# Performance work log

Hardware: AMD Instinct MI355X
Metric: run time of the kernel (lower is better)

Reference implementation:

```python
import jax, jax.numpy as jnp
import numpy as np

EMBED = 1024
HEADS = 16
HEAD_DIM = EMBED // HEADS


def setup_inputs() -> dict:
    key = jax.random.key(0)
    ks = jax.random.split(key, 8)
    b, t, d = 2, 2048, EMBED
    s = 1.0 / np.sqrt(d)
    return {
        'k': jax.random.normal(ks[0], (b, t, d), jnp.float32),
        'q': jax.random.normal(ks[1], (b, t, d), jnp.float32),
        'v': jax.random.normal(ks[2], (b, t, d), jnp.float32),
        'Wk': jax.random.normal(ks[3], (d, d), jnp.float32) * s,
        'Wq': jax.random.normal(ks[4], (d, d), jnp.float32) * s,
        'Wv': jax.random.normal(ks[5], (d, d), jnp.float32) * s,
        'Wo': jax.random.normal(ks[6], (d, d), jnp.float32) * s,
        'bo': jax.random.normal(ks[7], (d,), jnp.float32) * 0.01,
    }


def reference(k, q, v, Wk, Wq, Wv, Wo, bo):
    b, t, d = q.shape
    h, n = HEADS, HEAD_DIM
    # projections (q_prj bias=False, k/v bias=False per add_bias_kv=False)
    keys = (k @ Wk.T).reshape(b, t, h, n).transpose(0, 2, 1, 3)      # b h t n
    queries = (q @ Wq.T).reshape(b, t, h, n).transpose(0, 2, 1, 3)
    values = (v @ Wv.T).reshape(b, t, h, n).transpose(0, 2, 1, 3)
    att = jnp.einsum('bhtn,bhsn->bhts', queries, keys)               # b h t t
    att = jax.nn.softmax(att / np.sqrt(n), axis=-1)
    out = jnp.einsum('bhts,bhsn->bhtn', att, values)                 # b h t n
    out = out.transpose(0, 2, 1, 3).reshape(b, t, d)                 # b t (h n)
    return out @ Wo.T + bo
```

## Files before the change

### kernel.cpp

```cpp
#include <hip/hip_runtime.h>
#include <hip/hip_bf16.h>


typedef unsigned short u16;
typedef unsigned int   u32;
using short8 = __attribute__((ext_vector_type(8))) short;
using f32x4  = __attribute__((ext_vector_type(4))) float;

__device__ __forceinline__ u16 f2b(float f) {
    u32 u = __float_as_uint(f);
    u += 0x7FFFu + ((u >> 16) & 1u);
    return (u16)(u >> 16);
}
__device__ __forceinline__ u32 pack2(float lo, float hi) {
    union { __hip_bfloat162 h; u32 u; } c;
    c.h = __float22bfloat162_rn(make_float2(lo, hi));
    return c.u;
}
__device__ __forceinline__ float fexp2(float x) {
    return __builtin_amdgcn_exp2f(x);
}
__device__ __forceinline__ void gld_lds16(const u16* g, u16* l) {
    __builtin_amdgcn_global_load_lds(
        (const __attribute__((address_space(1))) void*)g,
        (__attribute__((address_space(3))) void*)l, 16, 0, 0);
}

__global__ __launch_bounds__(256) void convert_kernel(
    const float* s0, const float* s1, const float* s2, const float* s3,
    const float* s4, const float* s5, const float* s6,
    u16* d0, u16* d1, u16* d2, u16* d3, u16* d4, u16* d5, u16* d6)
{
    const int y = blockIdx.y;
    const float* s; u16* d; u32 n;
    switch (y) {
        case 0: s = s0; d = d0; n = 1048576; break;
        case 1: s = s1; d = d1; n = 1048576; break;
        case 2: s = s2; d = d2; n = 1048576; break;
        case 3: s = s3; d = d3; n = 262144; break;
        case 4: s = s4; d = d4; n = 262144; break;
        case 5: s = s5; d = d5; n = 262144; break;
        default: s = s6; d = d6; n = 262144; break;
    }
    for (u32 i = blockIdx.x * 256 + threadIdx.x; i < n; i += 256 * 1024) {
        float4 f = ((const float4*)s)[i];
        uint2 o; o.x = pack2(f.x, f.y); o.y = pack2(f.z, f.w);
        ((uint2*)d)[i] = o;
    }
}

template <int MODE>
__device__ __forceinline__ void gemm_core(
    const u16* __restrict__ A, const u16* __restrict__ B,
    void* __restrict__ C, const float* __restrict__ bias, float scale,
    u32 bm, u32 bn)
{
    constexpr u32 K = 1024;
    __shared__ u16 As[128 * 32];
    __shared__ u16 Bs[128 * 32];

    const int tid  = threadIdx.x;
    const int lane = tid & 63;
    const int w    = tid >> 6;
    const int wr   = w >> 1, wc = w & 1;
    const int ml   = lane & 15, g = lane >> 4;

    f32x4 acc[4][4] = {};

    const u32 srow = w * 32 + (lane >> 2);
    const u32 scol = (u32)(((lane & 3) ^ ((lane >> 3) & 3)) * 8);
    const u16* gA = A + (size_t)(bm + srow) * K + scol;
    const u16* gB = B + (size_t)(bn + srow) * K + scol;
    u16* lA = &As[w * 1024];
    u16* lB = &Bs[w * 1024];

    const u32 fsw = (u32)((g ^ ((ml >> 1) & 3)) * 8);

    for (u32 k0 = 0; k0 < K; k0 += 32) {
        __syncthreads();
        gld_lds16(gA + k0, lA);
        gld_lds16(gA + 16 * K + k0, lA + 512);
        gld_lds16(gB + k0, lB);
        gld_lds16(gB + 16 * K + k0, lB + 512);
        __syncthreads();

        short8 af[4], bf[4];
#pragma unroll
        for (int it = 0; it < 4; ++it)
            af[it] = *(const short8*)&As[(wr * 64 + it * 16 + ml) * 32 + fsw];
#pragma unroll
        for (int ct = 0; ct < 4; ++ct)
            bf[ct] = *(const short8*)&Bs[(wc * 64 + ct * 16 + ml) * 32 + fsw];
#pragma unroll
        for (int it = 0; it < 4; ++it)
#pragma unroll
            for (int ct = 0; ct < 4; ++ct)
                acc[it][ct] = __builtin_amdgcn_mfma_f32_16x16x32_bf16(
                    af[it], bf[ct], acc[it][ct], 0, 0, 0);
    }

    if (MODE == 3) {
#pragma unroll
        for (int ct = 0; ct < 4; ++ct) {
            const u32 col = bn + wc * 64 + ct * 16 + ml;
            u16* dst = (u16*)C + (col >> 11) * 2097152 + (col & 2047);
#pragma unroll
            for (int it = 0; it < 4; ++it) {
                const u32 row = bm + wr * 64 + it * 16 + g * 4;
#pragma unroll
                for (int r = 0; r < 4; ++r)
                    dst[(size_t)(row + r) * 2048] = f2b(acc[it][ct][r]);
            }
        }
    } else {
#pragma unroll
        for (int ct = 0; ct < 4; ++ct) {
            const u32 col = bn + wc * 64 + ct * 16 + ml;
            const float bv = (MODE == 2 && bias) ? bias[col] : 0.0f;
#pragma unroll
            for (int it = 0; it < 4; ++it) {
                const u32 row = bm + wr * 64 + it * 16 + g * 4;
#pragma unroll
                for (int r = 0; r < 4; ++r) {
                    const float v = acc[it][ct][r] * scale + bv;
                    if (MODE == 2) ((float*)C)[(size_t)(row + r) * 1024 + col] = v;
                    else           ((u16*)C)[(size_t)(row + r) * 1024 + col] = f2b(v);
                }
            }
        }
    }
}

__global__ __launch_bounds__(256) void proj3_kernel(
    const u16* kb, const u16* qb, const u16* vb,
    const u16* Wkb, const u16* Wqb, const u16* Wvb,
    u16* Kp, u16* Qp, u16* Vt)
{
    if (blockIdx.z == 0)
        gemm_core<0>(kb, Wkb, Kp, nullptr, 1.0f, blockIdx.y * 128, blockIdx.x * 128);
    else if (blockIdx.z == 1)
        gemm_core<0>(qb, Wqb, Qp, nullptr, 0.18033688011112042f, blockIdx.y * 128, blockIdx.x * 128);
    else
        gemm_core<3>(Wvb, vb, Vt, nullptr, 1.0f, blockIdx.x * 128, blockIdx.y * 128);
}

__global__ __launch_bounds__(256) void out_gemm_kernel(
    const u16* __restrict__ A, const u16* __restrict__ W,
    float* __restrict__ C, const float* __restrict__ bias)
{
    constexpr u32 K = 1024;
    __shared__ u16 As[64 * 32];
    __shared__ u16 Bs[128 * 32];

    const int tid  = threadIdx.x;
    const int lane = tid & 63;
    const int w    = tid >> 6;
    const int wr   = w >> 1, wc = w & 1;
    const int ml   = lane & 15, g = lane >> 4;
    const u32 bm   = blockIdx.y * 64, bn = blockIdx.x * 128;

    f32x4 acc[2][4] = {};

    const u32 scol = (u32)(((lane & 3) ^ ((lane >> 3) & 3)) * 8);
    const u16* gA = A + (size_t)(bm + w * 16 + (lane >> 2)) * K + scol;
    const u16* gB = W + (size_t)(bn + w * 32 + (lane >> 2)) * K + scol;
    u16* lA = &As[w * 512];
    u16* lB = &Bs[w * 1024];

    const u32 fsw = (u32)((g ^ ((ml >> 1) & 3)) * 8);

    for (u32 k0 = 0; k0 < K; k0 += 32) {
        __syncthreads();
        gld_lds16(gA + k0, lA);
        gld_lds16(gB + k0, lB);
        gld_lds16(gB + 16 * K + k0, lB + 512);
        __syncthreads();

        short8 af[2], bf[4];
#pragma unroll
        for (int it = 0; it < 2; ++it)
            af[it] = *(const short8*)&As[(wr * 32 + it * 16 + ml) * 32 + fsw];
#pragma unroll
        for (int ct = 0; ct < 4; ++ct)
            bf[ct] = *(const short8*)&Bs[(wc * 64 + ct * 16 + ml) * 32 + fsw];
#pragma unroll
        for (int it = 0; it < 2; ++it)
#pragma unroll
            for (int ct = 0; ct < 4; ++ct)
                acc[it][ct] = __builtin_amdgcn_mfma_f32_16x16x32_bf16(
                    af[it], bf[ct], acc[it][ct], 0, 0, 0);
    }

#pragma unroll
    for (int ct = 0; ct < 4; ++ct) {
        const u32 col = bn + wc * 64 + ct * 16 + ml;
        const float bv = bias ? bias[col] : 0.0f;
#pragma unroll
        for (int it = 0; it < 2; ++it) {
            const u32 row = bm + wr * 32 + it * 16 + g * 4;
#pragma unroll
            for (int r = 0; r < 4; ++r)
                C[(size_t)(row + r) * 1024 + col] = acc[it][ct][r] + bv;
        }
    }
}

__global__ __launch_bounds__(512, 4) void attn_kernel(
    const u16* __restrict__ Qp, const u16* __restrict__ Kp,
    const u16* __restrict__ Vt, u16* __restrict__ Op)
{
    __shared__ u16   Ks[2 * 4096];
    __shared__ u16   Vs[2 * 4096];
    __shared__ u16   Ps[8 * 1280];
    __shared__ float Ls[4][32];

    const int tid  = threadIdx.x;
    const int lane = tid & 63;
    const int w    = tid >> 6;
    const int wq   = w >> 1;
    const int ws   = w & 1;
    const int ml   = lane & 15;
    const int g    = lane >> 4;

    const u32 fid  = blockIdx.x + (blockIdx.y << 4);
    const u32 swz  = (fid & 7) * 64 + (fid >> 3);
    const u32 bh   = swz >> 4;
    const u32 t0   = (swz & 15) * 128;
    const u32 b    = bh >> 4, h = bh & 15;

    const u32 base  = b * 2048 * 1024 + h * 64;
    const u32 vbase = bh * 64 * 2048;

    short8 bq[2][2];
#pragma unroll
    for (int qt = 0; qt < 2; ++qt) {
        const u16* qr = Qp + base + (t0 + wq * 32 + qt * 16 + ml) * 1024 + g * 8;
        bq[qt][0] = *(const short8*)qr;
        bq[qt][1] = *(const short8*)(qr + 32);
    }

    f32x4 oacc[4][2] = {};
    float l4[2] = {};

    const u32 srow = (u32)(lane >> 3);
    const u32 schk = (u32)((lane & 7) ^ (lane >> 3));
    const u16* gK = Kp + base + (size_t)(w * 8 + srow) * 1024 + schk * 8;
    const u16* gV = Vt + vbase + (size_t)(w * 8 + srow) * 2048 + schk * 8;
    u16* lK0 = &Ks[w * 512];
    u16* lK1 = &Ks[4096 + w * 512];
    u16* lV0 = &Vs[w * 512];
    u16* lV1 = &Vs[4096 + w * 512];

    const u32 kaOff = (u32)((ws * 32 + ml) * 64 + ((g ^ (ml & 7)) * 8));
    const u32 vaOff = (u32)(ml * 64 + (((ws * 4 + g) ^ (ml & 7)) * 8));
    u16* Pw  = &Ps[w * 1280];
    u32* PwU = (u32*)Pw;
    const u32 pWr = (u32)(ml * 20 + g * 2);
    const u32 pRd = (u32)(ml * 40 + g * 8);

#define ATTN_STAGE(KD, VD)                                                   \
    { gld_lds16(gK, (KD)); gld_lds16(gV, (VD)); gK += 65536; gV += 64; }

#define ATTN_COMPUTE(KB, VB)                                                 \
    {                                                                        \
        __builtin_amdgcn_s_setprio(1);                                       \
        short8 vv[4];                                                        \
        _Pragma("unroll")                                                    \
        for (int dt = 0; dt < 4; ++dt)                                       \
            vv[dt] = *(const short8*)&(VB)[vaOff + dt * 1024];               \
        _Pragma("unroll")                                                    \
        for (int sub = 0; sub < 2; ++sub) {                                  \
            short8 k0 = *(const short8*)&(KB)[kaOff + sub * 1024];           \
            short8 k1 = *(const short8*)&(KB)[(kaOff ^ 32) + sub * 1024];    \
            _Pragma("unroll")                                                \
            for (int qt = 0; qt < 2; ++qt) {                                 \
                f32x4 z = {};                                                \
                z = __builtin_amdgcn_mfma_f32_16x16x32_bf16(                 \
                    k0, bq[qt][0], z, 0, 0, 0);                              \
                z = __builtin_amdgcn_mfma_f32_16x16x32_bf16(                 \
                    k1, bq[qt][1], z, 0, 0, 0);                              \
                const float p0 = fexp2(z[0]), p1 = fexp2(z[1]);              \
                const float p2 = fexp2(z[2]), p3 = fexp2(z[3]);              \
                l4[qt] += (p0 + p1) + (p2 + p3);                             \
                uint2 pv; pv.x = pack2(p0, p1); pv.y = pack2(p2, p3);        \
                *(uint2*)&PwU[pWr + (u32)(qt * 320 + sub * 8)] = pv;         \
            }                                                                \
        }                                                                    \
        _Pragma("unroll")                                                    \
        for (int qt = 0; qt < 2; ++qt) {                                     \
            short8 pb = *(const short8*)&Pw[pRd + (u32)(qt * 640)];          \
            _Pragma("unroll")                                                \
            for (int dt = 0; dt < 4; ++dt)                                   \
                oacc[dt][qt] = __builtin_amdgcn_mfma_f32_16x16x32_bf16(      \
                    vv[dt], pb, oacc[dt][qt], 0, 0, 0);                      \
        }                                                                    \
        __builtin_amdgcn_s_setprio(0);                                       \
    }

    ATTN_STAGE(lK0, lV0)
    __syncthreads();

#pragma unroll 1
    for (int it = 0; it < 16; ++it) {
        ATTN_STAGE(lK1, lV1)
        ATTN_COMPUTE(Ks, Vs)
        __syncthreads();
        if (it < 15) ATTN_STAGE(lK0, lV0)
        ATTN_COMPUTE(Ks + 4096, Vs + 4096)
        __syncthreads();
    }
#undef ATTN_STAGE
#undef ATTN_COMPUTE

#pragma unroll
    for (int qt = 0; qt < 2; ++qt) {
        l4[qt] += __shfl_xor(l4[qt], 16);
        l4[qt] += __shfl_xor(l4[qt], 32);
    }

    float* Rw = (wq < 2) ? ((float*)Ks + wq * 2048) : ((float*)Vs + (wq - 2) * 2048);
    if (ws == 1) {
#pragma unroll
        for (int dt = 0; dt < 4; ++dt)
#pragma unroll
            for (int qt = 0; qt < 2; ++qt)
#pragma unroll
                for (int r = 0; r < 4; ++r)
                    Rw[(dt * 16 + g * 4 + r) * 32 + qt * 16 + ml] = oacc[dt][qt][r];
        if (g == 0) {
#pragma unroll
            for (int qt = 0; qt < 2; ++qt) Ls[wq][qt * 16 + ml] = l4[qt];
        }
    }
    __syncthreads();
    if (ws == 0) {
#pragma unroll
        for (int dt = 0; dt < 4; ++dt)
#pragma unroll
            for (int qt = 0; qt < 2; ++qt)
#pragma unroll
                for (int r = 0; r < 4; ++r)
                    oacc[dt][qt][r] += Rw[(dt * 16 + g * 4 + r) * 32 + qt * 16 + ml];
#pragma unroll
        for (int qt = 0; qt < 2; ++qt) {
            const u32 q = (u32)(wq * 32 + qt * 16 + ml);
            const float inv = 1.0f / (l4[qt] + Ls[wq][qt * 16 + ml]);
            const u32 row = (b * 2048 + t0 + q) * 1024 + h * 64;
#pragma unroll
            for (int dt = 0; dt < 4; ++dt) {
                const u32 ci = row + dt * 16 + g * 4;
                *(u32*)&Op[ci]     = pack2(oacc[dt][qt][0] * inv, oacc[dt][qt][1] * inv);
                *(u32*)&Op[ci + 2] = pack2(oacc[dt][qt][2] * inv, oacc[dt][qt][3] * inv);
            }
        }
    }
}

extern "C" void kernel_launch(void* const* d_in, const int* in_sizes, int n_in,
                              void* d_out, int out_size, void* d_ws, size_t ws_size,
                              hipStream_t stream)
{
    const float* kin = (const float*)d_in[0];
    const float* qin = (const float*)d_in[1];
    const float* vin = (const float*)d_in[2];
    const float* Wk  = (const float*)d_in[3];
    const float* Wq  = (const float*)d_in[4];
    const float* Wv  = (const float*)d_in[5];
    const float* Wo  = (const float*)d_in[6];
    const float* bo  = (const float*)d_in[7];
    float* out = (float*)d_out;

    const size_t ACT = 4194304;
    const size_t WSZ = 1048576;

    u16* kb  = (u16*)d_ws;
    u16* qb  = kb + ACT;
    u16* vb  = qb + ACT;
    u16* Wkb = vb + ACT;
    u16* Wqb = Wkb + WSZ;
    u16* Wvb = Wqb + WSZ;
    u16* Wob = Wvb + WSZ;
    u16* Kp  = Wob + WSZ;
    u16* Qp  = Kp + ACT;
    u16* Vt  = Qp + ACT;
    u16* Op  = kb;

    convert_kernel<<<dim3(1024, 7), 256, 0, stream>>>(
        kin, qin, vin, Wk, Wq, Wv, Wo, kb, qb, vb, Wkb, Wqb, Wvb, Wob);
    proj3_kernel<<<dim3(8, 32, 3), 256, 0, stream>>>(
        kb, qb, vb, Wkb, Wqb, Wvb, Kp, Qp, Vt);
    attn_kernel<<<dim3(16, 32), 512, 0, stream>>>(Qp, Kp, Vt, Op);
    out_gemm_kernel<<<dim3(8, 64), 256, 0, stream>>>(Op, Wob, out, bo);
}
```

Before: 209.1 us.

## Fuse fp32-to-bf16 activation and Wo conversion into GEMM tile loads

The separate pass that converted k/q/v activations and Wo to bf16 is removed. The projection GEMM now reads fp32 tiles straight from global memory, packs them to bf16 in registers and writes them to LDS; the output GEMM does the same for Wo. A smaller kernel still converts Wk/Wq/Wv. This drops a full read-plus-write pass over about 48MB of activations, but each fp32 tile is now re-read (through L2) by every column block, and these loads go through registers instead of direct global-to-LDS loads.

New measurement: 231.7 us. +10.8%, slower.

```diff
diff --git a/kernel.cpp b/kernel.cpp
--- a/kernel.cpp
+++ b/kernel.cpp
@@ -26,34 +26,24 @@
         (__attribute__((address_space(3))) void*)l, 16, 0, 0);
 }
 
-__global__ __launch_bounds__(256) void convert_kernel(
-    const float* s0, const float* s1, const float* s2, const float* s3,
-    const float* s4, const float* s5, const float* s6,
-    u16* d0, u16* d1, u16* d2, u16* d3, u16* d4, u16* d5, u16* d6)
+__global__ __launch_bounds__(256) void convert_w_kernel(
+    const float* s0, const float* s1, const float* s2,
+    u16* d0, u16* d1, u16* d2)
 {
     const int y = blockIdx.y;
-    const float* s; u16* d; u32 n;
-    switch (y) {
-        case 0: s = s0; d = d0; n = 1048576; break;
-        case 1: s = s1; d = d1; n = 1048576; break;
-        case 2: s = s2; d = d2; n = 1048576; break;
-        case 3: s = s3; d = d3; n = 262144; break;
-        case 4: s = s4; d = d4; n = 262144; break;
-        case 5: s = s5; d = d5; n = 262144; break;
-        default: s = s6; d = d6; n = 262144; break;
-    }
-    for (u32 i = blockIdx.x * 256 + threadIdx.x; i < n; i += 256 * 1024) {
+    const float* s = (y == 0) ? s0 : ((y == 1) ? s1 : s2);
+    u16*         d = (y == 0) ? d0 : ((y == 1) ? d1 : d2);
+    for (u32 i = blockIdx.x * 256 + threadIdx.x; i < 262144; i += 256 * 256) {
         float4 f = ((const float4*)s)[i];
         uint2 o; o.x = pack2(f.x, f.y); o.y = pack2(f.z, f.w);
         ((uint2*)d)[i] = o;
     }
 }
 
-template <int MODE>
+template <int MODE, int AF32, int BF32>
 __device__ __forceinline__ void gemm_core(
-    const u16* __restrict__ A, const u16* __restrict__ B,
-    void* __restrict__ C, const float* __restrict__ bias, float scale,
-    u32 bm, u32 bn)
+    const void* __restrict__ Av, const void* __restrict__ Bv,
+    void* __restrict__ C, float scale, u32 bm, u32 bn)
 {
     constexpr u32 K = 1024;
     __shared__ u16 As[128 * 32];
@@ -69,19 +59,56 @@
 
     const u32 srow = w * 32 + (lane >> 2);
     const u32 scol = (u32)(((lane & 3) ^ ((lane >> 3) & 3)) * 8);
-    const u16* gA = A + (size_t)(bm + srow) * K + scol;
-    const u16* gB = B + (size_t)(bn + srow) * K + scol;
-    u16* lA = &As[w * 1024];
-    u16* lB = &Bs[w * 1024];
+    const u16*   gA  = (const u16*)Av   + (size_t)(bm + srow) * K + scol;
+    const float* gAf = (const float*)Av + (size_t)(bm + srow) * K + scol;
+    const u16*   gB  = (const u16*)Bv   + (size_t)(bn + srow) * K + scol;
+    const float* gBf = (const float*)Bv + (size_t)(bn + srow) * K + scol;
+    u16* lA  = &As[w * 1024];
+    u16* lB  = &Bs[w * 1024];
+    u16* lAw = &As[w * 1024 + (u32)(lane * 8)];
+    u16* lBw = &Bs[w * 1024 + (u32)(lane * 8)];
 
     const u32 fsw = (u32)((g ^ ((ml >> 1) & 3)) * 8);
 
     for (u32 k0 = 0; k0 < K; k0 += 32) {
-        __syncthreads();
-        gld_lds16(gA + k0, lA);
-        gld_lds16(gA + 16 * K + k0, lA + 512);
-        gld_lds16(gB + k0, lB);
-        gld_lds16(gB + 16 * K + k0, lB + 512);
+        float4 av4[4], bv4[4];
+        if constexpr (AF32) {
+            av4[0] = *(const float4*)(gAf + k0);
+            av4[1] = *(const float4*)(gAf + k0 + 4);
+            av4[2] = *(const float4*)(gAf + 16 * K + k0);
+            av4[3] = *(const float4*)(gAf + 16 * K + k0 + 4);
+        }
+        if constexpr (BF32) {
+            bv4[0] = *(const float4*)(gBf + k0);
+            bv4[1] = *(const float4*)(gBf + k0 + 4);
+            bv4[2] = *(const float4*)(gBf + 16 * K + k0);
+            bv4[3] = *(const float4*)(gBf + 16 * K + k0 + 4);
+        }
+        __syncthreads();
+        if constexpr (AF32) {
+            uint4 p0, p1;
+            p0.x = pack2(av4[0].x, av4[0].y); p0.y = pack2(av4[0].z, av4[0].w);
+            p0.z = pack2(av4[1].x, av4[1].y); p0.w = pack2(av4[1].z, av4[1].w);
+            p1.x = pack2(av4[2].x, av4[2].y); p1.y = pack2(av4[2].z, av4[2].w);
+            p1.z = pack2(av4[3].x, av4[3].y); p1.w = pack2(av4[3].z, av4[3].w);
+            *(uint4*)lAw = p0;
+            *(uint4*)(lAw + 512) = p1;
+        } else {
+            gld_lds16(gA + k0, lA);
+            gld_lds16(gA + 16 * K + k0, lA + 512);
+        }
+        if constexpr (BF32) {
+            uint4 p0, p1;
+            p0.x = pack2(bv4[0].x, bv4[0].y); p0.y = pack2(bv4[0].z, bv4[0].w);
+            p0.z = pack2(bv4[1].x, bv4[1].y); p0.w = pack2(bv4[1].z, bv4[1].w);
+            p1.x = pack2(bv4[2].x, bv4[2].y); p1.y = pack2(bv4[2].z, bv4[2].w);
+            p1.z = pack2(bv4[3].x, bv4[3].y); p1.w = pack2(bv4[3].z, bv4[3].w);
+            *(uint4*)lBw = p0;
+            *(uint4*)(lBw + 512) = p1;
+        } else {
+            gld_lds16(gB + k0, lB);
+            gld_lds16(gB + 16 * K + k0, lB + 512);
+        }
         __syncthreads();
 
         short8 af[4], bf[4];
@@ -116,36 +143,33 @@
 #pragma unroll
         for (int ct = 0; ct < 4; ++ct) {
             const u32 col = bn + wc * 64 + ct * 16 + ml;
-            const float bv = (MODE == 2 && bias) ? bias[col] : 0.0f;
 #pragma unroll
             for (int it = 0; it < 4; ++it) {
                 const u32 row = bm + wr * 64 + it * 16 + g * 4;
 #pragma unroll
-                for (int r = 0; r < 4; ++r) {
-                    const float v = acc[it][ct][r] * scale + bv;
-                    if (MODE == 2) ((float*)C)[(size_t)(row + r) * 1024 + col] = v;
-                    else           ((u16*)C)[(size_t)(row + r) * 1024 + col] = f2b(v);
-                }
+                for (int r = 0; r < 4; ++r)
+                    ((u16*)C)[(size_t)(row + r) * 1024 + col] =
+                        f2b(acc[it][ct][r] * scale);
             }
         }
     }
 }
 
 __global__ __launch_bounds__(256) void proj3_kernel(
-    const u16* kb, const u16* qb, const u16* vb,
+    const float* kin, const float* qin, const float* vin,
     const u16* Wkb, const u16* Wqb, const u16* Wvb,
     u16* Kp, u16* Qp, u16* Vt)
 {
     if (blockIdx.z == 0)
-        gemm_core<0>(kb, Wkb, Kp, nullptr, 1.0f, blockIdx.y * 128, blockIdx.x * 128);
+        gemm_core<0, 1, 0>(kin, Wkb, Kp, 1.0f, blockIdx.y * 128, blockIdx.x * 128);
     else if (blockIdx.z == 1)
-        gemm_core<0>(qb, Wqb, Qp, nullptr, 0.18033688011112042f, blockIdx.y * 128, blockIdx.x * 128);
+        gemm_core<0, 1, 0>(qin, Wqb, Qp, 0.18033688011112042f, blockIdx.y * 128, blockIdx.x * 128);
     else
-        gemm_core<3>(Wvb, vb, Vt, nullptr, 1.0f, blockIdx.x * 128, blockIdx.y * 128);
+        gemm_core<3, 0, 1>(Wvb, vin, Vt, 1.0f, blockIdx.x * 128, blockIdx.y * 128);
 }
 
 __global__ __launch_bounds__(256) void out_gemm_kernel(
-    const u16* __restrict__ A, const u16* __restrict__ W,
+    const u16* __restrict__ A, const float* __restrict__ W,
     float* __restrict__ C, const float* __restrict__ bias)
 {
     constexpr u32 K = 1024;
@@ -162,18 +186,30 @@
     f32x4 acc[2][4] = {};
 
     const u32 scol = (u32)(((lane & 3) ^ ((lane >> 3) & 3)) * 8);
-    const u16* gA = A + (size_t)(bm + w * 16 + (lane >> 2)) * K + scol;
-    const u16* gB = W + (size_t)(bn + w * 32 + (lane >> 2)) * K + scol;
-    u16* lA = &As[w * 512];
-    u16* lB = &Bs[w * 1024];
+    const u16*   gA  = A + (size_t)(bm + w * 16 + (lane >> 2)) * K + scol;
+    const float* gBf = W + (size_t)(bn + w * 32 + (lane >> 2)) * K + scol;
+    u16* lA  = &As[w * 512];
+    u16* lBw = &Bs[w * 1024 + (u32)(lane * 8)];
 
     const u32 fsw = (u32)((g ^ ((ml >> 1) & 3)) * 8);
 
     for (u32 k0 = 0; k0 < K; k0 += 32) {
+        float4 bv4[4];
+        bv4[0] = *(const float4*)(gBf + k0);
+        bv4[1] = *(const float4*)(gBf + k0 + 4);
+        bv4[2] = *(const float4*)(gBf + 16 * K + k0);
+        bv4[3] = *(const float4*)(gBf + 16 * K + k0 + 4);
         __syncthreads();
         gld_lds16(gA + k0, lA);
-        gld_lds16(gB + k0, lB);
-        gld_lds16(gB + 16 * K + k0, lB + 512);
+        {
+            uint4 p0, p1;
+            p0.x = pack2(bv4[0].x, bv4[0].y); p0.y = pack2(bv4[0].z, bv4[0].w);
+            p0.z = pack2(bv4[1].x, bv4[1].y); p0.w = pack2(bv4[1].z, bv4[1].w);
+            p1.x = pack2(bv4[2].x, bv4[2].y); p1.y = pack2(bv4[2].z, bv4[2].w);
+            p1.z = pack2(bv4[3].x, bv4[3].y); p1.w = pack2(bv4[3].z, bv4[3].w);
+            *(uint4*)lBw = p0;
+            *(uint4*)(lBw + 512) = p1;
+        }
         __syncthreads();
 
         short8 af[2], bf[4];
@@ -385,10 +421,10 @@
     u16* Vt  = Qp + ACT;
     u16* Op  = kb;
 
-    convert_kernel<<<dim3(1024, 7), 256, 0, stream>>>(
-        kin, qin, vin, Wk, Wq, Wv, Wo, kb, qb, vb, Wkb, Wqb, Wvb, Wob);
+    convert_w_kernel<<<dim3(256, 3), 256, 0, stream>>>(
+        Wk, Wq, Wv, Wkb, Wqb, Wvb);
     proj3_kernel<<<dim3(8, 32, 3), 256, 0, stream>>>(
-        kb, qb, vb, Wkb, Wqb, Wvb, Kp, Qp, Vt);
+        kin, qin, vin, Wkb, Wqb, Wvb, Kp, Qp, Vt);
     attn_kernel<<<dim3(16, 32), 512, 0, stream>>>(Qp, Kp, Vt, Op);
-    out_gemm_kernel<<<dim3(8, 64), 256, 0, stream>>>(Op, Wob, out, bo);
-}
+    out_gemm_kernel<<<dim3(8, 64), 256, 0, stream>>>(Op, Wo, out, bo);
+}
```
